# Kernel optimization log

Hardware: AMD Instinct MI355X
Metric: run time of the kernel (lower is better)

Reference implementation:

```python
import jax, jax.numpy as jnp
import numpy as np

# dims: B batch, T timesteps, V nodes, D in-features, C channels, d pos-emb dim,
# TS = t_size (spatio-temporal window), P prediction steps, L layers (=4, fixed by GLU(C*4))
B, T, V, D, C, d, TS, P, L = 4, 12, 512, 1, 64, 8, 3, 12, 4
BETA = TS - 1


def setup_inputs() -> dict:
    key = jax.random.key(0)
    ks = jax.random.split(key, 30)
    n = lambda i, shape, s=1.0: jax.random.normal(ks[i], shape, dtype=jnp.float32) * s
    return dict(
        x=n(0, (B, T, V, D)),
        sape=n(1, (V, d)),
        tape=n(2, (B, T, 1, d)),
        srpe=n(3, (V, V, d)),
        trpe=n(4, (TS, 1, d)),
        zeros_x=jnp.zeros((B, BETA, V, C), jnp.float32),
        zeros_tape=jnp.zeros((B, BETA, 1, d), jnp.float32),
        range_mask=(jax.random.uniform(ks[5], (B, V, TS * V)) < 0.5).astype(jnp.float32),
        Wi=n(6, (D, C), D ** -0.5), bi=n(7, (C,), 0.02),
        gc_mu=n(8, (L, 6, d)), gc_sig=n(9, (L, 6, d), 0.5),
        Wg=n(10, (L, C, 2 * C), C ** -0.5), bg=n(11, (L, 2 * C), 0.02),
        Wsp=n(12, (L, d, 2 * C), d ** -0.5), Wtp=n(13, (L, d, 2 * C), d ** -0.5),
        fs_w=n(14, (L, C, C, T), (C * T) ** -0.5), fs_b=n(15, (L, C), 0.02),
        glu1_w=n(16, (L, 2 * C, C), C ** -0.5), glu1_b=n(17, (L, 2 * C), 0.02),
        gout_w=n(18, (8 * C, 4 * C), (4 * C) ** -0.5), gout_b=n(19, (8 * C,), 0.02),
        out_w=n(20, (P, 4 * C), (4 * C) ** -0.5), out_b=n(21, (P,), 0.02),
    )


def _glu_cv(w, b, y):
    # 1x1-conv GLU over channel dim of y: (B, Cin, V) -> (B, Cin, V)
    z = jnp.einsum('oc,bcv->bov', w, y) + b[None, :, None]
    zl, zr = jnp.split(z, 2, axis=1)
    return zl * jax.nn.sigmoid(zr)


def _forward(x, sape, tape, srpe, trpe, Wi, bi, gc_mu, gc_sig, Wg, bg, Wsp, Wtp,
             fs_w, fs_b, glu1_w, glu1_b, gout_w, gout_b, out_w, out_b,
             zeros_x, zeros_tape, range_mask):
    b_, t_ = x.shape[0], x.shape[1]
    v_ = sape.shape[0]
    ts = trpe.shape[0]
    widx = jnp.arange(t_)[:, None] + jnp.arange(ts)  # (T, t_size) sliding-window indices
    h = x @ Wi + bi                                   # InputLayer: B,T,V,C
    tape_pad = jnp.concatenate([zeros_tape, tape], axis=1)  # B,T+beta,1,d
    skips = []
    for l in range(gc_mu.shape[0]):
        mu, sig = gc_mu[l], gc_sig[l]
        gc = lambda emb, i: jnp.sum(-0.5 * (emb - mu[i]) ** 2 * sig[i] ** 2, axis=-1)
        # STPRI: Gaussian position-aware relation inference
        base = gc(sape, 0)[:, None] + gc(sape, 1)[None, :] + gc(srpe, 4)        # (V_i, V_j)
        per_t = gc(tape, 2)[:, :, 0][:, :, None] \
              + gc(tape_pad, 3)[:, :, 0][:, widx] \
              + gc(trpe, 5)[:, 0]                                               # B,T,t_size
        S = jnp.exp(per_t[:, :, :, None, None] + base)                          # B,T,k,i,j (<=1, safe)
        S = S.transpose(0, 1, 4, 2, 3).reshape(b_, t_, v_, ts * v_)             # B,T,j,(k*V+i)
        S = S * range_mask[:, None]                                             # masked relations
        # STPGConv: masked graph conv over the t_size*V window + gating
        x_pad = jnp.concatenate([zeros_x, h], axis=1)                           # B,T+beta,V,C
        xw = x_pad[:, widx].reshape(b_, t_, ts * v_, -1)                        # B,T,t_size*V,C
        g = jnp.einsum('btjm,btmc->btjc', S, xw) @ Wg[l] + bg[l]                # B,T,V,2C
        g = g + sape @ Wsp[l] + tape @ Wtp[l]                                   # +SE(V,2C) +TE(B,T,1,2C)
        gl, gr = jnp.split(g, 2, axis=-1)
        h = gl * jax.nn.sigmoid(gr)                                             # B,T,V,C
        # GFS: conv over time (kernel (1,T)) + GLU -> B,C,V
        y = jnp.einsum('bcvt,oct->bov', h.transpose(0, 3, 2, 1), fs_w[l]) + fs_b[l][None, :, None]
        skips.append(_glu_cv(glu1_w[l], glu1_b[l], y))
    s = _glu_cv(gout_w, gout_b, jnp.concatenate(skips, axis=1))                  # B,4C,V
    return jnp.einsum('oc,bcv->bov', out_w, s) + out_b[None, :, None]            # B,P,V


def reference(x, sape, tape, srpe, trpe, zeros_x, zeros_tape, range_mask, Wi, bi,
              gc_mu, gc_sig, Wg, bg, Wsp, Wtp, fs_w, fs_b, glu1_w, glu1_b,
              gout_w, gout_b, out_w, out_b):
    return _forward(x, sape, tape, srpe, trpe, Wi, bi, gc_mu, gc_sig, Wg, bg, Wsp, Wtp,
                    fs_w, fs_b, glu1_w, glu1_b, gout_w, gout_b, out_w, out_b,
                    zeros_x, zeros_tape, range_mask)
```

## Files before the change

kernel.cpp:

```cpp
#include <hip/hip_runtime.h>
#include <math.h>


typedef unsigned short u16;
typedef __attribute__((ext_vector_type(8))) short short8;
typedef __attribute__((ext_vector_type(4))) float f32x4;
typedef __attribute__((ext_vector_type(8))) unsigned short u16x8;
typedef __attribute__((ext_vector_type(4))) unsigned short u16x4;

#define MFMA16(a, b, c) __builtin_amdgcn_mfma_f32_16x16x32_bf16((a), (b), (c), 0, 0, 0)

__device__ __forceinline__ float b2f(u16 u) {
  union { unsigned int i; float f; } x; x.i = ((unsigned int)u) << 16; return x.f;
}
__device__ __forceinline__ u16 f2b(float f) {
  union { float f; unsigned int i; } x; x.f = f;
  unsigned int r = x.i + 0x7FFFu + ((x.i >> 16) & 1u);
  return (u16)(r >> 16);
}
__device__ __forceinline__ void ld8f(const float* __restrict__ p, float* f) {
  f32x4 a = *(const f32x4*)p;
  f32x4 b = *(const f32x4*)(p + 4);
  #pragma unroll
  for (int i = 0; i < 4; ++i) { f[i] = a[i]; f[4 + i] = b[i]; }
}
__device__ __forceinline__ float gcf(const float* e, const float* __restrict__ mu,
                                     const float* __restrict__ sg) {
  float s = 0.f;
  #pragma unroll
  for (int i = 0; i < 8; ++i) {
    float dm = e[i] - mu[i];
    s += dm * dm * sg[i] * sg[i];
  }
  return -0.5f * s;
}
__device__ __forceinline__ float sigm(float v) { return 1.0f / (1.0f + expf(-v)); }

__global__ __launch_bounds__(256) void prep_kernel(
    const float* __restrict__ x, const float* __restrict__ sape,
    const float* __restrict__ tape, const float* __restrict__ srpe,
    const float* __restrict__ trpe, const float* __restrict__ Wi,
    const float* __restrict__ bi, const float* __restrict__ gmu,
    const float* __restrict__ gsg, const float* __restrict__ Wg,
    const float* __restrict__ bg, const float* __restrict__ Wsp,
    const float* __restrict__ Wtp, const float* __restrict__ fsw,
    const float* __restrict__ mask,
    const float* __restrict__ g1w, const float* __restrict__ gw,
    const float* __restrict__ ow,
    u16* __restrict__ hT0, u16* __restrict__ Abf,
    float* __restrict__ spb, float* __restrict__ tpb,
    u16* __restrict__ fswT, u16* __restrict__ WgT, float* __restrict__ ev,
    u16* __restrict__ g1wB, u16* __restrict__ gwB, u16* __restrict__ owB) {
  const int tid = threadIdx.x;
  int bid = blockIdx.x;

  if (bid < 768) {
    int gid = bid * 256 + tid;
    int i8 = gid & 63, c = (gid >> 6) & 63, bt = gid >> 12;
    float xv[8];
    ld8f(&x[bt * 512 + i8 * 8], xv);
    float wic = Wi[c], bic = bi[c];
    u16x8 hv;
    #pragma unroll
    for (int ii = 0; ii < 8; ++ii) hv[ii] = f2b(xv[ii] * wic + bic);
    *(u16x8*)&hT0[gid * 8] = hv;
    return;
  }
  bid -= 768;
  if (bid < 1024) {
    int gid = bid * 256 + tid;
    int i = gid & 511, j = gid >> 9;
    float fi[8], fj[8], fr[8];
    ld8f(sape + i * 8, fi);
    ld8f(sape + j * 8, fj);
    ld8f(srpe + ((size_t)i * 512 + j) * 8, fr);
    u16 eb[4];
    #pragma unroll
    for (int l = 0; l < 4; ++l) {
      const float* mub = gmu + l * 48;
      const float* sgb = gsg + l * 48;
      float s = gcf(fi, mub + 0, sgb + 0)
              + gcf(fj, mub + 8, sgb + 8)
              + gcf(fr, mub + 32, sgb + 32);
      eb[l] = f2b(expf(s));
    }
    #pragma unroll
    for (int b = 0; b < 4; ++b)
      #pragma unroll
      for (int k = 0; k < 3; ++k) {
        float mv = mask[((size_t)(b * 512 + j)) * 1536 + k * 512 + i];
        u16 m = (mv != 0.f) ? (u16)0xFFFFu : (u16)0;
        #pragma unroll
        for (int l = 0; l < 4; ++l)
          Abf[((size_t)((l * 4 + b) * 512 + j)) * 1536 + k * 512 + i] = eb[l] & m;
      }
    return;
  }
  bid -= 1024;
  if (bid < 1024) {
    int gid = bid * 256 + tid;
    int o = gid & 127, j = (gid >> 7) & 511, l = gid >> 16;
    float s = 0.f;
    #pragma unroll
    for (int dd = 0; dd < 8; ++dd)
      s += sape[j * 8 + dd] * Wsp[(l * 8 + dd) * 128 + o];
    spb[gid] = s;
    return;
  }
  bid -= 1024;
  if (bid < 96) {
    int gid = bid * 256 + tid;
    int o = gid & 127, bt = (gid >> 7) % 48, l = gid / 6144;
    float s = bg[l * 128 + o];
    #pragma unroll
    for (int dd = 0; dd < 8; ++dd)
      s += tape[bt * 8 + dd] * Wtp[(l * 8 + dd) * 128 + o];
    tpb[gid] = s;
    return;
  }
  bid -= 96;
  if (bid < 768) {
    int gid = bid * 256 + tid;
    int kidx = gid % 768, rest = gid / 768;
    int o = rest & 63, l = rest >> 6;
    int c = kidx & 63, tt = kidx >> 6;
    fswT[gid] = f2b(fsw[((l * 64 + o) * 64 + c) * 12 + tt]);
    return;
  }
  bid -= 768;
  if (bid < 128) {
    int gid = bid * 256 + tid;
    int c = gid & 63, o = (gid >> 6) & 127, l = gid >> 13;
    WgT[gid] = f2b(Wg[(l * 64 + c) * 128 + o]);
    return;
  }
  bid -= 128;
  if (bid < 3) {
    int gid = bid * 256 + tid;
    if (gid < 576) {
      int k = gid % 3, t = (gid / 3) % 12, b = (gid / 36) % 4, l = gid / 144;
      const float* mub = gmu + l * 48;
      const float* sgb = gsg + l * 48;
      float e2[8], e3[8], e5[8];
      ld8f(tape + (b * 12 + t) * 8, e2);
      int tp = t + k - 2;
      if (tp >= 0) ld8f(tape + (b * 12 + tp) * 8, e3);
      else {
        #pragma unroll
        for (int ii = 0; ii < 8; ++ii) e3[ii] = 0.f;
      }
      ld8f(trpe + k * 8, e5);
      float s = gcf(e2, mub + 16, sgb + 16)
              + gcf(e3, mub + 24, sgb + 24)
              + gcf(e5, mub + 40, sgb + 40);
      ev[gid] = expf(s);
    }
    return;
  }
  bid -= 3;
  if (bid < 128) {
    int gid = bid * 256 + tid;
    g1wB[gid] = f2b(g1w[gid]);
    return;
  }
  bid -= 128;
  if (bid < 512) {
    int gid = bid * 256 + tid;
    gwB[gid] = f2b(gw[gid]);
    return;
  }
  bid -= 512;
  {
    int gid = bid * 256 + tid;
    if (gid < 3072) owB[gid] = f2b(ow[gid]);
  }
}

__global__ __launch_bounds__(256) void agg_kernel(
    const u16* __restrict__ Abfl, const u16* __restrict__ hT,
    u16* __restrict__ G) {
  __shared__ u16 As[128][72];
  __shared__ u16 Bs[128][72];
  const int tid = threadIdx.x, wid = tid >> 6, lane = tid & 63;
  const int l16 = lane & 15, quad = lane >> 4;
  const int bid = blockIdx.x;
  const int nt = bid / 48;
  const int rest = bid % 48;
  const int mt = rest & 3;
  const int k  = (rest >> 2) % 3;
  const int b  = rest / 12;
  const int wm = wid >> 1, wn = wid & 1;

  const u16* Arow0 = Abfl + ((size_t)(b * 512 + mt * 128)) * 1536 + k * 512;
  f32x4 acc[4][4] = {};

  for (int it = 0; it < 8; ++it) {
    const int i0 = it * 64;
    #pragma unroll
    for (int s = 0; s < 4; ++s) {
      int idx = s * 256 + tid;
      int r = idx >> 3, ch = (idx & 7) * 8;
      *(u16x8*)&As[r][ch] = *(const u16x8*)&Arow0[(size_t)r * 1536 + i0 + ch];
      int tp = nt * 2 + (r >> 6), c = r & 63;
      *(u16x8*)&Bs[r][ch] =
          *(const u16x8*)&hT[((size_t)((b * 12 + tp) * 64 + c)) * 512 + i0 + ch];
    }
    __syncthreads();
    #pragma unroll
    for (int ks = 0; ks < 2; ++ks) {
      short8 af[4], bf[4];
      #pragma unroll
      for (int mb = 0; mb < 4; ++mb)
        af[mb] = *(const short8*)&As[wm * 64 + mb * 16 + l16][ks * 32 + quad * 8];
      #pragma unroll
      for (int nb = 0; nb < 4; ++nb)
        bf[nb] = *(const short8*)&Bs[wn * 64 + nb * 16 + l16][ks * 32 + quad * 8];
      #pragma unroll
      for (int mb = 0; mb < 4; ++mb)
        #pragma unroll
        for (int nb = 0; nb < 4; ++nb)
          acc[mb][nb] = MFMA16(af[mb], bf[nb], acc[mb][nb]);
    }
    __syncthreads();
  }

  u16* base = &As[0][0];
  #pragma unroll
  for (int mb = 0; mb < 4; ++mb)
    #pragma unroll
    for (int nb = 0; nb < 4; ++nb) {
      int n = wn * 64 + nb * 16 + l16;
      #pragma unroll
      for (int r = 0; r < 4; ++r) {
        int m = wm * 64 + mb * 16 + quad * 4 + r;
        base[m * 128 + n] = f2b(acc[mb][nb][r]);
      }
    }
  __syncthreads();
  u16* Gp = G + ((size_t)((b * 3 + k) * 512 + mt * 128)) * 768 + nt * 128;
  #pragma unroll
  for (int s = 0; s < 8; ++s) {
    int idx = s * 256 + tid;
    int m = idx >> 4, ch = (idx & 15) * 8;
    *(u16x8*)&Gp[(size_t)m * 768 + ch] = *(const u16x8*)&base[m * 128 + ch];
  }
}

__global__ __launch_bounds__(256) void combine_kernel(
    const u16* __restrict__ G, const float* __restrict__ evl,
    const u16* __restrict__ WgTl, const float* __restrict__ spbl,
    const float* __restrict__ tpbl, const u16* __restrict__ fswTl,
    u16* __restrict__ hTout, u16* __restrict__ yptl) {
  __shared__ u16 aggL[128][72];
  __shared__ u16 hL[128][72];
  const int tid = threadIdx.x, wid = tid >> 6, lane = tid & 63;
  const int l16 = lane & 15, quad = lane >> 4;
  const int bid = blockIdx.x;
  const int mt = bid & 3;
  const int bt = bid >> 2;
  const int b = bt / 12, t = bt - b * 12;

  {
    int j = tid >> 1;
    int c0 = (tid & 1) * 32;
    float accv[32];
    #pragma unroll
    for (int ii = 0; ii < 32; ++ii) accv[ii] = 0.f;
    #pragma unroll
    for (int k = 0; k < 3; ++k) {
      int tp = t + k - 2;
      if (tp < 0) continue;
      float ek = evl[bt * 3 + k];
      const u16* gp = &G[((size_t)((b * 3 + k) * 512 + mt * 128 + j)) * 768 + tp * 64 + c0];
      #pragma unroll
      for (int s = 0; s < 4; ++s) {
        u16x8 gv = *(const u16x8*)&gp[s * 8];
        #pragma unroll
        for (int ii = 0; ii < 8; ++ii) accv[s * 8 + ii] += b2f(gv[ii]) * ek;
      }
    }
    #pragma unroll
    for (int s = 0; s < 4; ++s) {
      u16x8 ov;
      #pragma unroll
      for (int ii = 0; ii < 8; ++ii) ov[ii] = f2b(accv[s * 8 + ii]);
      *(u16x8*)&aggL[j][c0 + s * 8] = ov;
    }
  }
  __syncthreads();

  f32x4 acc2[8][2] = {};
  #pragma unroll
  for (int ks = 0; ks < 2; ++ks) {
    short8 bf[2];
    #pragma unroll
    for (int nb = 0; nb < 2; ++nb)
      bf[nb] = *(const short8*)&aggL[wid * 32 + nb * 16 + l16][ks * 32 + quad * 8];
    #pragma unroll
    for (int mb = 0; mb < 8; ++mb) {
      short8 a = *(const short8*)&WgTl[(mb * 16 + l16) * 64 + ks * 32 + quad * 8];
      acc2[mb][0] = MFMA16(a, bf[0], acc2[mb][0]);
      acc2[mb][1] = MFMA16(a, bf[1], acc2[mb][1]);
    }
  }

  #pragma unroll
  for (int mb = 0; mb < 4; ++mb) {
    int ob = mb * 16 + quad * 4;
    #pragma unroll
    for (int nb = 0; nb < 2; ++nb) {
      int jl = wid * 32 + nb * 16 + l16;
      int jg = mt * 128 + jl;
      f32x4 spl = *(const f32x4*)&spbl[jg * 128 + ob];
      f32x4 spr = *(const f32x4*)&spbl[jg * 128 + 64 + ob];
      f32x4 tpl = *(const f32x4*)&tpbl[bt * 128 + ob];
      f32x4 tpr = *(const f32x4*)&tpbl[bt * 128 + 64 + ob];
      #pragma unroll
      for (int r = 0; r < 4; ++r) {
        float vl = acc2[mb][nb][r] + spl[r] + tpl[r];
        float vr = acc2[mb + 4][nb][r] + spr[r] + tpr[r];
        u16 hb = f2b(vl * sigm(vr));
        hTout[((size_t)((b * 12 + t) * 64 + ob + r)) * 512 + jg] = hb;
        hL[jl][ob + r] = hb;
      }
    }
  }
  __syncthreads();

  f32x4 accY[4][2] = {};
  #pragma unroll
  for (int ks = 0; ks < 2; ++ks) {
    short8 bfv[2];
    #pragma unroll
    for (int nb = 0; nb < 2; ++nb)
      bfv[nb] = *(const short8*)&hL[wid * 32 + nb * 16 + l16][ks * 32 + quad * 8];
    #pragma unroll
    for (int mb = 0; mb < 4; ++mb) {
      short8 a = *(const short8*)&fswTl[(mb * 16 + l16) * 768 + t * 64 + ks * 32 + quad * 8];
      accY[mb][0] = MFMA16(a, bfv[0], accY[mb][0]);
      accY[mb][1] = MFMA16(a, bfv[1], accY[mb][1]);
    }
  }
  #pragma unroll
  for (int mb = 0; mb < 4; ++mb)
    #pragma unroll
    for (int nb = 0; nb < 2; ++nb) {
      int j = mt * 128 + wid * 32 + nb * 16 + l16;
      #pragma unroll
      for (int r = 0; r < 4; ++r) {
        int o = mb * 16 + quad * 4 + r;
        yptl[((size_t)(bt * 64 + o)) * 512 + j] = f2b(accY[mb][nb][r]);
      }
    }
}

__global__ __launch_bounds__(256) void reduce_kernel(
    const u16* __restrict__ ypt, const float* __restrict__ fsb,
    u16* __restrict__ yB) {
  int gid = blockIdx.x * 256 + threadIdx.x;
  int j4 = gid & 127, o = (gid >> 7) & 63, b = (gid >> 13) & 3, l = gid >> 15;
  const u16* base = &ypt[(size_t)l * 1572864 +
                         ((size_t)((b * 12) * 64 + o)) * 512 + j4 * 4];
  float fb = fsb[l * 64 + o];
  f32x4 s = {fb, fb, fb, fb};
  #pragma unroll
  for (int t = 0; t < 12; ++t) {
    u16x4 v = *(const u16x4*)&base[(size_t)t * 32768];
    #pragma unroll
    for (int ii = 0; ii < 4; ++ii) s[ii] += b2f(v[ii]);
  }
  u16x4 pk;
  #pragma unroll
  for (int ii = 0; ii < 4; ++ii) pk[ii] = f2b(s[ii]);
  *(u16x4*)&yB[((size_t)((l * 4 + b) * 64 + o)) * 512 + j4 * 4] = pk;
}

__global__ __launch_bounds__(256) void glu1cat_kernel(
    const u16* __restrict__ yB, const u16* __restrict__ g1wB,
    const float* __restrict__ g1b, u16* __restrict__ catB) {
  __shared__ u16 yL[128][72];
  const int tid = threadIdx.x, wid = tid >> 6, lane = tid & 63;
  const int l16 = lane & 15, quad = lane >> 4;
  const int l = blockIdx.x >> 4;
  const int b = (blockIdx.x >> 2) & 3;
  const int v0 = (blockIdx.x & 3) * 128;

  {
    int o = tid & 63, sv = tid >> 6;
    const u16* src = &yB[((size_t)((l * 4 + b) * 64 + o)) * 512 + v0 + sv * 32];
    u16x8 p0 = *(const u16x8*)&src[0];
    u16x8 p1 = *(const u16x8*)&src[8];
    u16x8 p2 = *(const u16x8*)&src[16];
    u16x8 p3 = *(const u16x8*)&src[24];
    #pragma unroll
    for (int ii = 0; ii < 8; ++ii) {
      yL[sv * 32 + ii][o] = p0[ii];
      yL[sv * 32 + 8 + ii][o] = p1[ii];
      yL[sv * 32 + 16 + ii][o] = p2[ii];
      yL[sv * 32 + 24 + ii][o] = p3[ii];
    }
  }
  __syncthreads();

  f32x4 acc[2][8] = {};
  #pragma unroll
  for (int ks = 0; ks < 2; ++ks) {
    short8 a0 = *(const short8*)&g1wB[l * 8192 + (wid * 16 + l16) * 64 +
                                      ks * 32 + quad * 8];
    short8 a1 = *(const short8*)&g1wB[l * 8192 + (64 + wid * 16 + l16) * 64 +
                                      ks * 32 + quad * 8];
    #pragma unroll
    for (int nb = 0; nb < 8; ++nb) {
      short8 bf = *(const short8*)&yL[nb * 16 + l16][ks * 32 + quad * 8];
      acc[0][nb] = MFMA16(a0, bf, acc[0][nb]);
      acc[1][nb] = MFMA16(a1, bf, acc[1][nb]);
    }
  }
  #pragma unroll
  for (int nb = 0; nb < 8; ++nb) {
    int v = v0 + nb * 16 + l16;
    int oc = wid * 16 + quad * 4;
    u16x4 pk;
    #pragma unroll
    for (int r = 0; r < 4; ++r) {
      float zl = acc[0][nb][r] + g1b[l * 128 + oc + r];
      float zr = acc[1][nb][r] + g1b[l * 128 + 64 + oc + r];
      pk[r] = f2b(zl * sigm(zr));
    }
    *(u16x4*)&catB[((size_t)(b * 512 + v)) * 256 + l * 64 + oc] = pk;
  }
}

__global__ __launch_bounds__(256) void gout_kernel(
    const u16* __restrict__ catB, const u16* __restrict__ gwB,
    const float* __restrict__ gb, u16* __restrict__ sB) {
  __shared__ u16 cL[64][264];
  const int tid = threadIdx.x, wid = tid >> 6, lane = tid & 63;
  const int l16 = lane & 15, quad = lane >> 4;
  const int wm = wid >> 1, wn = wid & 1;
  const int b = blockIdx.x >> 6;
  const int v0 = ((blockIdx.x >> 3) & 7) * 64;
  const int cc0 = (blockIdx.x & 7) * 32;

  {
    int v = tid >> 2, seg = (tid & 3) * 64;
    const u16* src = &catB[((size_t)(b * 512 + v0 + v)) * 256 + seg];
    #pragma unroll
    for (int s = 0; s < 8; ++s)
      *(u16x8*)&cL[v][seg + s * 8] = *(const u16x8*)&src[s * 8];
  }
  __syncthreads();

  f32x4 acc[2][2] = {};
  #pragma unroll
  for (int ks = 0; ks < 8; ++ks) {
    short8 aL = *(const short8*)&gwB[(cc0 + wm * 16 + l16) * 256 +
                                     ks * 32 + quad * 8];
    short8 aH = *(const short8*)&gwB[(256 + cc0 + wm * 16 + l16) * 256 +
                                     ks * 32 + quad * 8];
    #pragma unroll
    for (int nb = 0; nb < 2; ++nb) {
      short8 bf = *(const short8*)&cL[wn * 32 + nb * 16 + l16][ks * 32 + quad * 8];
      acc[0][nb] = MFMA16(aL, bf, acc[0][nb]);
      acc[1][nb] = MFMA16(aH, bf, acc[1][nb]);
    }
  }
  #pragma unroll
  for (int nb = 0; nb < 2; ++nb) {
    int v = v0 + wn * 32 + nb * 16 + l16;
    int cc = cc0 + wm * 16 + quad * 4;
    u16x4 pk;
    #pragma unroll
    for (int r = 0; r < 4; ++r) {
      float zl = acc[0][nb][r] + gb[cc + r];
      float zr = acc[1][nb][r] + gb[256 + cc + r];
      pk[r] = f2b(zl * sigm(zr));
    }
    *(u16x4*)&sB[((size_t)(b * 512 + v)) * 256 + cc] = pk;
  }
}

__global__ __launch_bounds__(256) void head_kernel(
    const u16* __restrict__ sB, const u16* __restrict__ owB,
    const float* __restrict__ obv, float* __restrict__ out) {
  const int tid = threadIdx.x, wid = tid >> 6, lane = tid & 63;
  const int l16 = lane & 15, quad = lane >> 4;
  const int b = blockIdx.x >> 3;
  const int v0 = (blockIdx.x & 7) * 64;

  f32x4 acc = {};
  #pragma unroll
  for (int ks = 0; ks < 8; ++ks) {
    short8 a;
    if (l16 < 12) a = *(const short8*)&owB[l16 * 256 + ks * 32 + quad * 8];
    else {
      #pragma unroll
      for (int ii = 0; ii < 8; ++ii) a[ii] = 0;
    }
    short8 bf = *(const short8*)&sB[((size_t)(b * 512 + v0 + wid * 16 + l16)) * 256 +
                                    ks * 32 + quad * 8];
    acc = MFMA16(a, bf, acc);
  }
  #pragma unroll
  for (int r = 0; r < 4; ++r) {
    int p = quad * 4 + r;
    if (p < 12)
      out[(b * 12 + p) * 512 + v0 + wid * 16 + l16] = acc[r] + obv[p];
  }
}

extern "C" void kernel_launch(void* const* d_in, const int* in_sizes, int n_in,
                              void* d_out, int out_size, void* d_ws, size_t ws_size,
                              hipStream_t stream) {
  const float* x    = (const float*)d_in[0];
  const float* sape = (const float*)d_in[1];
  const float* tape = (const float*)d_in[2];
  const float* srpe = (const float*)d_in[3];
  const float* trpe = (const float*)d_in[4];
  const float* mask = (const float*)d_in[7];
  const float* Wi   = (const float*)d_in[8];
  const float* bi   = (const float*)d_in[9];
  const float* gmu  = (const float*)d_in[10];
  const float* gsg  = (const float*)d_in[11];
  const float* Wg   = (const float*)d_in[12];
  const float* bg   = (const float*)d_in[13];
  const float* Wsp  = (const float*)d_in[14];
  const float* Wtp  = (const float*)d_in[15];
  const float* fsw  = (const float*)d_in[16];
  const float* fsb  = (const float*)d_in[17];
  const float* g1w  = (const float*)d_in[18];
  const float* g1b  = (const float*)d_in[19];
  const float* gow  = (const float*)d_in[20];
  const float* gob  = (const float*)d_in[21];
  const float* ow   = (const float*)d_in[22];
  const float* obv  = (const float*)d_in[23];

  char* w = (char*)d_ws;
  u16*   hT_a = (u16*)(w + 0);
  u16*   hT_b = (u16*)(w + 3145728);
  u16*   Abf  = (u16*)(w + 6291456);
  u16*   G    = (u16*)(w + 31457280);
  u16*   fswT = (u16*)(w + 40894464);
  u16*   WgT  = (u16*)(w + 41287680);
  u16*   g1wB = (u16*)(w + 41353216);
  u16*   gwB  = (u16*)(w + 41418752);
  u16*   owB  = (u16*)(w + 41680896);
  float* spb  = (float*)(w + 41689088);
  float* tpb  = (float*)(w + 42737664);
  float* ev   = (float*)(w + 42835968);
  u16*   ypt  = (u16*)(w + 42852352);
  u16*   yB   = (u16*)(w + 55435264);
  u16*   catB = (u16*)(w + 57532416);
  u16*   sB   = (u16*)(w + 58580992);

  prep_kernel<<<4463, 256, 0, stream>>>(x, sape, tape, srpe, trpe, Wi, bi, gmu, gsg,
                                        Wg, bg, Wsp, Wtp, fsw, mask, g1w, gow, ow,
                                        hT_a, Abf, spb, tpb, fswT, WgT, ev,
                                        g1wB, gwB, owB);
  u16* hin = hT_a;
  u16* hout = hT_b;
  for (int l = 0; l < 4; ++l) {
    agg_kernel<<<288, 256, 0, stream>>>(Abf + (size_t)l * 3145728, hin, G);
    combine_kernel<<<192, 256, 0, stream>>>(G, ev + l * 144, WgT + l * 8192,
                                            spb + l * 65536, tpb + l * 6144,
                                            fswT + l * 49152, hout,
                                            ypt + (size_t)l * 1572864);
    u16* tmp = hin; hin = hout; hout = tmp;
  }
  reduce_kernel<<<512, 256, 0, stream>>>(ypt, fsb, yB);
  glu1cat_kernel<<<64, 256, 0, stream>>>(yB, g1wB, g1b, catB);
  gout_kernel<<<256, 256, 0, stream>>>(catB, gwB, gob, sB);
  head_kernel<<<32, 256, 0, stream>>>(sB, owB, obv, (float*)d_out);
}
```

Baseline: 239.0 us.

## Fuse GLU1, output GLU and head into a single tail kernel

Replaces the three final kernels (per-layer GLU producing the concatenated skips, the output GLU, and the prediction head) with one kernel. Each block handles 32 nodes of one batch and keeps intermediates in shared memory. This removes two kernel launches and the global writes and reads of the catB and sB buffers. In exchange, the output GLU stage runs on only 64 blocks instead of 256, and each block streams the full gout weight matrix, which lowers parallelism.

```diff
diff --git a/kernel.cpp b/kernel.cpp
--- a/kernel.cpp
+++ b/kernel.cpp
@@ -375,137 +375,121 @@
   *(u16x4*)&yB[((size_t)((l * 4 + b) * 64 + o)) * 512 + j4 * 4] = pk;
 }
 
-__global__ __launch_bounds__(256) void glu1cat_kernel(
+__global__ __launch_bounds__(256) void tail_kernel(
     const u16* __restrict__ yB, const u16* __restrict__ g1wB,
-    const float* __restrict__ g1b, u16* __restrict__ catB) {
-  __shared__ u16 yL[128][72];
+    const float* __restrict__ g1b, const u16* __restrict__ gwB,
+    const float* __restrict__ gb, const u16* __restrict__ owB,
+    const float* __restrict__ obv, float* __restrict__ out) {
+  __shared__ u16 yT[32][280];
+  __shared__ u16 catL[32][264];
   const int tid = threadIdx.x, wid = tid >> 6, lane = tid & 63;
   const int l16 = lane & 15, quad = lane >> 4;
-  const int l = blockIdx.x >> 4;
-  const int b = (blockIdx.x >> 2) & 3;
-  const int v0 = (blockIdx.x & 3) * 128;
+  const int b = blockIdx.x >> 4;
+  const int v0 = (blockIdx.x & 15) * 32;
 
   {
-    int o = tid & 63, sv = tid >> 6;
-    const u16* src = &yB[((size_t)((l * 4 + b) * 64 + o)) * 512 + v0 + sv * 32];
-    u16x8 p0 = *(const u16x8*)&src[0];
-    u16x8 p1 = *(const u16x8*)&src[8];
-    u16x8 p2 = *(const u16x8*)&src[16];
-    u16x8 p3 = *(const u16x8*)&src[24];
-    #pragma unroll
-    for (int ii = 0; ii < 8; ++ii) {
-      yL[sv * 32 + ii][o] = p0[ii];
-      yL[sv * 32 + 8 + ii][o] = p1[ii];
-      yL[sv * 32 + 16 + ii][o] = p2[ii];
-      yL[sv * 32 + 24 + ii][o] = p3[ii];
+    const int l = wid, o = lane;
+    const u16* src = &yB[((size_t)((l * 4 + b) * 64 + o)) * 512 + v0];
+    #pragma unroll
+    for (int s = 0; s < 4; ++s) {
+      u16x8 p = *(const u16x8*)&src[s * 8];
+      #pragma unroll
+      for (int ii = 0; ii < 8; ++ii) yT[s * 8 + ii][l * 64 + o] = p[ii];
     }
   }
   __syncthreads();
 
-  f32x4 acc[2][8] = {};
-  #pragma unroll
-  for (int ks = 0; ks < 2; ++ks) {
-    short8 a0 = *(const short8*)&g1wB[l * 8192 + (wid * 16 + l16) * 64 +
-                                      ks * 32 + quad * 8];
-    short8 a1 = *(const short8*)&g1wB[l * 8192 + (64 + wid * 16 + l16) * 64 +
-                                      ks * 32 + quad * 8];
-    #pragma unroll
-    for (int nb = 0; nb < 8; ++nb) {
-      short8 bf = *(const short8*)&yL[nb * 16 + l16][ks * 32 + quad * 8];
-      acc[0][nb] = MFMA16(a0, bf, acc[0][nb]);
-      acc[1][nb] = MFMA16(a1, bf, acc[1][nb]);
-    }
-  }
-  #pragma unroll
-  for (int nb = 0; nb < 8; ++nb) {
-    int v = v0 + nb * 16 + l16;
-    int oc = wid * 16 + quad * 4;
-    u16x4 pk;
+  {
+    f32x4 accA[8][2] = {};
+    #pragma unroll
+    for (int ks = 0; ks < 2; ++ks) {
+      short8 bf[2];
+      #pragma unroll
+      for (int nb = 0; nb < 2; ++nb)
+        bf[nb] = *(const short8*)&yT[nb * 16 + l16][wid * 64 + ks * 32 + quad * 8];
+      #pragma unroll
+      for (int mb = 0; mb < 8; ++mb) {
+        short8 a = *(const short8*)&g1wB[wid * 8192 + (mb * 16 + l16) * 64 +
+                                         ks * 32 + quad * 8];
+        accA[mb][0] = MFMA16(a, bf[0], accA[mb][0]);
+        accA[mb][1] = MFMA16(a, bf[1], accA[mb][1]);
+      }
+    }
+    #pragma unroll
+    for (int mb = 0; mb < 4; ++mb) {
+      int oc = mb * 16 + quad * 4;
+      #pragma unroll
+      for (int nb = 0; nb < 2; ++nb) {
+        int v = nb * 16 + l16;
+        #pragma unroll
+        for (int r = 0; r < 4; ++r) {
+          float zl = accA[mb][nb][r] + g1b[wid * 128 + oc + r];
+          float zr = accA[mb + 4][nb][r] + g1b[wid * 128 + 64 + oc + r];
+          catL[v][wid * 64 + oc + r] = f2b(zl * sigm(zr));
+        }
+      }
+    }
+  }
+  __syncthreads();
+
+  u16* sL = &yT[0][0];
+  {
+    const int cc0 = wid * 64;
+    f32x4 accB[8][2] = {};
+    #pragma unroll
+    for (int ks = 0; ks < 8; ++ks) {
+      short8 bf[2];
+      #pragma unroll
+      for (int nb = 0; nb < 2; ++nb)
+        bf[nb] = *(const short8*)&catL[nb * 16 + l16][ks * 32 + quad * 8];
+      #pragma unroll
+      for (int mb = 0; mb < 4; ++mb) {
+        short8 aL = *(const short8*)&gwB[(size_t)(cc0 + mb * 16 + l16) * 256 +
+                                         ks * 32 + quad * 8];
+        short8 aH = *(const short8*)&gwB[(size_t)(256 + cc0 + mb * 16 + l16) * 256 +
+                                         ks * 32 + quad * 8];
+        accB[mb][0] = MFMA16(aL, bf[0], accB[mb][0]);
+        accB[mb][1] = MFMA16(aL, bf[1], accB[mb][1]);
+        accB[mb + 4][0] = MFMA16(aH, bf[0], accB[mb + 4][0]);
+        accB[mb + 4][1] = MFMA16(aH, bf[1], accB[mb + 4][1]);
+      }
+    }
+    #pragma unroll
+    for (int mb = 0; mb < 4; ++mb) {
+      int cc = cc0 + mb * 16 + quad * 4;
+      #pragma unroll
+      for (int nb = 0; nb < 2; ++nb) {
+        int v = nb * 16 + l16;
+        #pragma unroll
+        for (int r = 0; r < 4; ++r) {
+          float zl = accB[mb][nb][r] + gb[cc + r];
+          float zr = accB[mb + 4][nb][r] + gb[256 + cc + r];
+          sL[v * 264 + cc + r] = f2b(zl * sigm(zr));
+        }
+      }
+    }
+  }
+  __syncthreads();
+
+  if (wid < 2) {
+    f32x4 acc3 = {};
+    #pragma unroll
+    for (int ks = 0; ks < 8; ++ks) {
+      short8 a;
+      if (l16 < 12) a = *(const short8*)&owB[l16 * 256 + ks * 32 + quad * 8];
+      else {
+        #pragma unroll
+        for (int ii = 0; ii < 8; ++ii) a[ii] = 0;
+      }
+      short8 bf = *(const short8*)&sL[(wid * 16 + l16) * 264 + ks * 32 + quad * 8];
+      acc3 = MFMA16(a, bf, acc3);
+    }
     #pragma unroll
     for (int r = 0; r < 4; ++r) {
-      float zl = acc[0][nb][r] + g1b[l * 128 + oc + r];
-      float zr = acc[1][nb][r] + g1b[l * 128 + 64 + oc + r];
-      pk[r] = f2b(zl * sigm(zr));
-    }
-    *(u16x4*)&catB[((size_t)(b * 512 + v)) * 256 + l * 64 + oc] = pk;
-  }
-}
-
-__global__ __launch_bounds__(256) void gout_kernel(
-    const u16* __restrict__ catB, const u16* __restrict__ gwB,
-    const float* __restrict__ gb, u16* __restrict__ sB) {
-  __shared__ u16 cL[64][264];
-  const int tid = threadIdx.x, wid = tid >> 6, lane = tid & 63;
-  const int l16 = lane & 15, quad = lane >> 4;
-  const int wm = wid >> 1, wn = wid & 1;
-  const int b = blockIdx.x >> 6;
-  const int v0 = ((blockIdx.x >> 3) & 7) * 64;
-  const int cc0 = (blockIdx.x & 7) * 32;
-
-  {
-    int v = tid >> 2, seg = (tid & 3) * 64;
-    const u16* src = &catB[((size_t)(b * 512 + v0 + v)) * 256 + seg];
-    #pragma unroll
-    for (int s = 0; s < 8; ++s)
-      *(u16x8*)&cL[v][seg + s * 8] = *(const u16x8*)&src[s * 8];
-  }
-  __syncthreads();
-
-  f32x4 acc[2][2] = {};
-  #pragma unroll
-  for (int ks = 0; ks < 8; ++ks) {
-    short8 aL = *(const short8*)&gwB[(cc0 + wm * 16 + l16) * 256 +
-                                     ks * 32 + quad * 8];
-    short8 aH = *(const short8*)&gwB[(256 + cc0 + wm * 16 + l16) * 256 +
-                                     ks * 32 + quad * 8];
-    #pragma unroll
-    for (int nb = 0; nb < 2; ++nb) {
-      short8 bf = *(const short8*)&cL[wn * 32 + nb * 16 + l16][ks * 32 + quad * 8];
-      acc[0][nb] = MFMA16(aL, bf, acc[0][nb]);
-      acc[1][nb] = MFMA16(aH, bf, acc[1][nb]);
-    }
-  }
-  #pragma unroll
-  for (int nb = 0; nb < 2; ++nb) {
-    int v = v0 + wn * 32 + nb * 16 + l16;
-    int cc = cc0 + wm * 16 + quad * 4;
-    u16x4 pk;
-    #pragma unroll
-    for (int r = 0; r < 4; ++r) {
-      float zl = acc[0][nb][r] + gb[cc + r];
-      float zr = acc[1][nb][r] + gb[256 + cc + r];
-      pk[r] = f2b(zl * sigm(zr));
-    }
-    *(u16x4*)&sB[((size_t)(b * 512 + v)) * 256 + cc] = pk;
-  }
-}
-
-__global__ __launch_bounds__(256) void head_kernel(
-    const u16* __restrict__ sB, const u16* __restrict__ owB,
-    const float* __restrict__ obv, float* __restrict__ out) {
-  const int tid = threadIdx.x, wid = tid >> 6, lane = tid & 63;
-  const int l16 = lane & 15, quad = lane >> 4;
-  const int b = blockIdx.x >> 3;
-  const int v0 = (blockIdx.x & 7) * 64;
-
-  f32x4 acc = {};
-  #pragma unroll
-  for (int ks = 0; ks < 8; ++ks) {
-    short8 a;
-    if (l16 < 12) a = *(const short8*)&owB[l16 * 256 + ks * 32 + quad * 8];
-    else {
-      #pragma unroll
-      for (int ii = 0; ii < 8; ++ii) a[ii] = 0;
-    }
-    short8 bf = *(const short8*)&sB[((size_t)(b * 512 + v0 + wid * 16 + l16)) * 256 +
-                                    ks * 32 + quad * 8];
-    acc = MFMA16(a, bf, acc);
-  }
-  #pragma unroll
-  for (int r = 0; r < 4; ++r) {
-    int p = quad * 4 + r;
-    if (p < 12)
-      out[(b * 12 + p) * 512 + v0 + wid * 16 + l16] = acc[r] + obv[p];
+      int p = quad * 4 + r;
+      if (p < 12)
+        out[(b * 12 + p) * 512 + v0 + wid * 16 + l16] = acc3[r] + obv[p];
+    }
   }
 }
 
@@ -550,8 +534,6 @@
   float* ev   = (float*)(w + 42835968);
   u16*   ypt  = (u16*)(w + 42852352);
   u16*   yB   = (u16*)(w + 55435264);
-  u16*   catB = (u16*)(w + 57532416);
-  u16*   sB   = (u16*)(w + 58580992);
 
   prep_kernel<<<4463, 256, 0, stream>>>(x, sape, tape, srpe, trpe, Wi, bi, gmu, gsg,
                                         Wg, bg, Wsp, Wtp, fsw, mask, g1w, gow, ow,
@@ -568,7 +550,6 @@
     u16* tmp = hin; hin = hout; hout = tmp;
   }
   reduce_kernel<<<512, 256, 0, stream>>>(ypt, fsb, yB);
-  glu1cat_kernel<<<64, 256, 0, stream>>>(yB, g1wB, g1b, catB);
-  gout_kernel<<<256, 256, 0, stream>>>(catB, gwB, gob, sB);
-  head_kernel<<<32, 256, 0, stream>>>(sB, owB, obv, (float*)d_out);
-}
+  tail_kernel<<<64, 256, 0, stream>>>(yB, g1wB, g1b, gwB, gob, owB, obv,
+                                      (float*)d_out);
+}
```

New measurement: 241.5 us. Within noise of the previous version (+1.0%).

## Factor masked adjacency into per-layer base and shared bf16 mask, apply in agg load

Applied to the files above, without the earlier changes.

Prep no longer materializes the full masked adjacency (L×B×V×3V bf16, about 25MB) with scattered strided writes. It writes a per-layer base matrix (L×V×V) and a 16-bit mask (B×3×V×V, shared across layers) with vectorized stores. The aggregation kernel loads both tiles and ANDs them when filling shared memory. Prep write traffic drops a lot, at the cost of two global loads per A tile in each of the four aggregation launches.

```diff
diff --git a/kernel.cpp b/kernel.cpp
--- a/kernel.cpp
+++ b/kernel.cpp
@@ -47,7 +47,7 @@
     const float* __restrict__ mask,
     const float* __restrict__ g1w, const float* __restrict__ gw,
     const float* __restrict__ ow,
-    u16* __restrict__ hT0, u16* __restrict__ Abf,
+    u16* __restrict__ hT0, u16* __restrict__ ebase, u16* __restrict__ mask16,
     float* __restrict__ spb, float* __restrict__ tpb,
     u16* __restrict__ fswT, u16* __restrict__ WgT, float* __restrict__ ev,
     u16* __restrict__ g1wB, u16* __restrict__ gwB, u16* __restrict__ owB) {
@@ -74,7 +74,6 @@
     ld8f(sape + i * 8, fi);
     ld8f(sape + j * 8, fj);
     ld8f(srpe + ((size_t)i * 512 + j) * 8, fr);
-    u16 eb[4];
     #pragma unroll
     for (int l = 0; l < 4; ++l) {
       const float* mub = gmu + l * 48;
@@ -82,21 +81,24 @@
       float s = gcf(fi, mub + 0, sgb + 0)
               + gcf(fj, mub + 8, sgb + 8)
               + gcf(fr, mub + 32, sgb + 32);
-      eb[l] = f2b(expf(s));
-    }
-    #pragma unroll
-    for (int b = 0; b < 4; ++b)
-      #pragma unroll
-      for (int k = 0; k < 3; ++k) {
-        float mv = mask[((size_t)(b * 512 + j)) * 1536 + k * 512 + i];
-        u16 m = (mv != 0.f) ? (u16)0xFFFFu : (u16)0;
-        #pragma unroll
-        for (int l = 0; l < 4; ++l)
-          Abf[((size_t)((l * 4 + b) * 512 + j)) * 1536 + k * 512 + i] = eb[l] & m;
-      }
+      ebase[l * 262144 + j * 512 + i] = f2b(expf(s));
+    }
     return;
   }
   bid -= 1024;
+  if (bid < 1536) {
+    int gid = bid * 256 + tid;
+    int i8 = gid & 63, j = (gid >> 6) & 511, bk = gid >> 15;
+    int k = bk % 3, b = bk / 3;
+    float mv[8];
+    ld8f(&mask[((size_t)(b * 512 + j)) * 1536 + k * 512 + i8 * 8], mv);
+    u16x8 out;
+    #pragma unroll
+    for (int ii = 0; ii < 8; ++ii) out[ii] = (mv[ii] != 0.f) ? (u16)0xFFFFu : (u16)0;
+    *(u16x8*)&mask16[(size_t)gid * 8] = out;
+    return;
+  }
+  bid -= 1536;
   if (bid < 1024) {
     int gid = bid * 256 + tid;
     int o = gid & 127, j = (gid >> 7) & 511, l = gid >> 16;
@@ -177,8 +179,8 @@
 }
 
 __global__ __launch_bounds__(256) void agg_kernel(
-    const u16* __restrict__ Abfl, const u16* __restrict__ hT,
-    u16* __restrict__ G) {
+    const u16* __restrict__ ebl, const u16* __restrict__ m16,
+    const u16* __restrict__ hT, u16* __restrict__ G) {
   __shared__ u16 As[128][72];
   __shared__ u16 Bs[128][72];
   const int tid = threadIdx.x, wid = tid >> 6, lane = tid & 63;
@@ -191,7 +193,8 @@
   const int b  = rest / 12;
   const int wm = wid >> 1, wn = wid & 1;
 
-  const u16* Arow0 = Abfl + ((size_t)(b * 512 + mt * 128)) * 1536 + k * 512;
+  const u16* Erow0 = ebl + (size_t)(mt * 128) * 512;
+  const u16* Mrow0 = m16 + ((size_t)((b * 3 + k) * 512 + mt * 128)) * 512;
   f32x4 acc[4][4] = {};
 
   for (int it = 0; it < 8; ++it) {
@@ -200,7 +203,9 @@
     for (int s = 0; s < 4; ++s) {
       int idx = s * 256 + tid;
       int r = idx >> 3, ch = (idx & 7) * 8;
-      *(u16x8*)&As[r][ch] = *(const u16x8*)&Arow0[(size_t)r * 1536 + i0 + ch];
+      u16x8 ev8 = *(const u16x8*)&Erow0[(size_t)r * 512 + i0 + ch];
+      u16x8 mv8 = *(const u16x8*)&Mrow0[(size_t)r * 512 + i0 + ch];
+      *(u16x8*)&As[r][ch] = ev8 & mv8;
       int tp = nt * 2 + (r >> 6), c = r & 63;
       *(u16x8*)&Bs[r][ch] =
           *(const u16x8*)&hT[((size_t)((b * 12 + tp) * 64 + c)) * 512 + i0 + ch];
@@ -536,31 +541,32 @@
   const float* obv  = (const float*)d_in[23];
 
   char* w = (char*)d_ws;
-  u16*   hT_a = (u16*)(w + 0);
-  u16*   hT_b = (u16*)(w + 3145728);
-  u16*   Abf  = (u16*)(w + 6291456);
-  u16*   G    = (u16*)(w + 31457280);
-  u16*   fswT = (u16*)(w + 40894464);
-  u16*   WgT  = (u16*)(w + 41287680);
-  u16*   g1wB = (u16*)(w + 41353216);
-  u16*   gwB  = (u16*)(w + 41418752);
-  u16*   owB  = (u16*)(w + 41680896);
-  float* spb  = (float*)(w + 41689088);
-  float* tpb  = (float*)(w + 42737664);
-  float* ev   = (float*)(w + 42835968);
-  u16*   ypt  = (u16*)(w + 42852352);
-  u16*   yB   = (u16*)(w + 55435264);
-  u16*   catB = (u16*)(w + 57532416);
-  u16*   sB   = (u16*)(w + 58580992);
-
-  prep_kernel<<<4463, 256, 0, stream>>>(x, sape, tape, srpe, trpe, Wi, bi, gmu, gsg,
+  u16*   hT_a   = (u16*)(w + 0);
+  u16*   hT_b   = (u16*)(w + 3145728);
+  u16*   ebase  = (u16*)(w + 6291456);
+  u16*   mask16 = (u16*)(w + 8388608);
+  u16*   G      = (u16*)(w + 14680064);
+  u16*   fswT   = (u16*)(w + 24117248);
+  u16*   WgT    = (u16*)(w + 24510464);
+  u16*   g1wB   = (u16*)(w + 24576000);
+  u16*   gwB    = (u16*)(w + 24641536);
+  u16*   owB    = (u16*)(w + 24903680);
+  float* spb    = (float*)(w + 24911872);
+  float* tpb    = (float*)(w + 25960448);
+  float* ev     = (float*)(w + 26058752);
+  u16*   ypt    = (u16*)(w + 26075136);
+  u16*   yB     = (u16*)(w + 38658048);
+  u16*   catB   = (u16*)(w + 40755200);
+  u16*   sB     = (u16*)(w + 41803776);
+
+  prep_kernel<<<5999, 256, 0, stream>>>(x, sape, tape, srpe, trpe, Wi, bi, gmu, gsg,
                                         Wg, bg, Wsp, Wtp, fsw, mask, g1w, gow, ow,
-                                        hT_a, Abf, spb, tpb, fswT, WgT, ev,
+                                        hT_a, ebase, mask16, spb, tpb, fswT, WgT, ev,
                                         g1wB, gwB, owB);
   u16* hin = hT_a;
   u16* hout = hT_b;
   for (int l = 0; l < 4; ++l) {
-    agg_kernel<<<288, 256, 0, stream>>>(Abf + (size_t)l * 3145728, hin, G);
+    agg_kernel<<<288, 256, 0, stream>>>(ebase + (size_t)l * 262144, mask16, hin, G);
     combine_kernel<<<192, 256, 0, stream>>>(G, ev + l * 144, WgT + l * 8192,
                                             spb + l * 65536, tpb + l * 6144,
                                             fswT + l * 49152, hout,
```

Result: no change. 241.0 us (+0.8%).

## Double-buffer agg_kernel tiles with direct global-to-LDS loads and XOR swizzle

Applied to the files above, without the earlier changes.

Replaces the register-staged global-to-shared copy in agg_kernel with __builtin_amdgcn_global_load_lds, which writes straight into LDS. Shared tiles are now double-buffered so the next K-slice loads while MFMAs run on the current one. The unpadded 64-wide rows use an XOR swizzle on 16-byte slots to avoid bank conflicts. This doubles LDS use per block and relies on the single barrier per iteration to order the async LDS writes correctly.

```diff
diff --git a/kernel.cpp b/kernel.cpp
--- a/kernel.cpp
+++ b/kernel.cpp
@@ -35,6 +35,12 @@
   return -0.5f * s;
 }
 __device__ __forceinline__ float sigm(float v) { return 1.0f / (1.0f + expf(-v)); }
+
+__device__ __forceinline__ void gload16(const u16* g, u16* l) {
+  __builtin_amdgcn_global_load_lds(
+      (const __attribute__((address_space(1))) void*)g,
+      (__attribute__((address_space(3))) void*)l, 16, 0, 0);
+}
 
 __global__ __launch_bounds__(256) void prep_kernel(
     const float* __restrict__ x, const float* __restrict__ sape,
@@ -179,8 +185,8 @@
 __global__ __launch_bounds__(256) void agg_kernel(
     const u16* __restrict__ Abfl, const u16* __restrict__ hT,
     u16* __restrict__ G) {
-  __shared__ u16 As[128][72];
-  __shared__ u16 Bs[128][72];
+  __shared__ u16 As[2][128][64];
+  __shared__ u16 Bs[2][128][64];
   const int tid = threadIdx.x, wid = tid >> 6, lane = tid & 63;
   const int l16 = lane & 15, quad = lane >> 4;
   const int bid = blockIdx.x;
@@ -192,39 +198,56 @@
   const int wm = wid >> 1, wn = wid & 1;
 
   const u16* Arow0 = Abfl + ((size_t)(b * 512 + mt * 128)) * 1536 + k * 512;
+  const int srow = lane >> 3, sslot = lane & 7;
+
+  const u16* gaQ[4];
+  const u16* gbQ[4];
+  #pragma unroll
+  for (int q = 0; q < 4; ++q) {
+    int r = (wid * 4 + q) * 8 + srow;
+    gaQ[q] = Arow0 + (size_t)r * 1536 + ((sslot ^ (r & 7)) << 3);
+    int tp = nt * 2 + (r >> 6), c = r & 63;
+    gbQ[q] = hT + ((size_t)((b * 12 + tp) * 64 + c)) * 512 + ((sslot ^ (r & 7)) << 3);
+  }
+
   f32x4 acc[4][4] = {};
 
+  auto stage = [&](int bf, int i0) {
+    #pragma unroll
+    for (int q = 0; q < 4; ++q) {
+      gload16(gaQ[q] + i0, &As[bf][(wid * 4 + q) * 8][0]);
+      gload16(gbQ[q] + i0, &Bs[bf][(wid * 4 + q) * 8][0]);
+    }
+  };
+
+  stage(0, 0);
+  __syncthreads();
   for (int it = 0; it < 8; ++it) {
-    const int i0 = it * 64;
-    #pragma unroll
-    for (int s = 0; s < 4; ++s) {
-      int idx = s * 256 + tid;
-      int r = idx >> 3, ch = (idx & 7) * 8;
-      *(u16x8*)&As[r][ch] = *(const u16x8*)&Arow0[(size_t)r * 1536 + i0 + ch];
-      int tp = nt * 2 + (r >> 6), c = r & 63;
-      *(u16x8*)&Bs[r][ch] =
-          *(const u16x8*)&hT[((size_t)((b * 12 + tp) * 64 + c)) * 512 + i0 + ch];
-    }
-    __syncthreads();
+    const int cur = it & 1;
+    if (it < 7) stage(cur ^ 1, (it + 1) * 64);
     #pragma unroll
     for (int ks = 0; ks < 2; ++ks) {
-      short8 af[4], bf[4];
-      #pragma unroll
-      for (int mb = 0; mb < 4; ++mb)
-        af[mb] = *(const short8*)&As[wm * 64 + mb * 16 + l16][ks * 32 + quad * 8];
-      #pragma unroll
-      for (int nb = 0; nb < 4; ++nb)
-        bf[nb] = *(const short8*)&Bs[wn * 64 + nb * 16 + l16][ks * 32 + quad * 8];
+      short8 af[4], bfv[4];
+      #pragma unroll
+      for (int mb = 0; mb < 4; ++mb) {
+        int row = wm * 64 + mb * 16 + l16;
+        af[mb] = *(const short8*)&As[cur][row][((ks * 4 + quad) ^ (row & 7)) << 3];
+      }
+      #pragma unroll
+      for (int nb = 0; nb < 4; ++nb) {
+        int row = wn * 64 + nb * 16 + l16;
+        bfv[nb] = *(const short8*)&Bs[cur][row][((ks * 4 + quad) ^ (row & 7)) << 3];
+      }
       #pragma unroll
       for (int mb = 0; mb < 4; ++mb)
         #pragma unroll
         for (int nb = 0; nb < 4; ++nb)
-          acc[mb][nb] = MFMA16(af[mb], bf[nb], acc[mb][nb]);
+          acc[mb][nb] = MFMA16(af[mb], bfv[nb], acc[mb][nb]);
     }
     __syncthreads();
   }
 
-  u16* base = &As[0][0];
+  u16* base = &As[0][0][0];
   #pragma unroll
   for (int mb = 0; mb < 4; ++mb)
     #pragma unroll
```

After: 241.5 us. No clear change (+1.0%).
